# Kernel tuning notes

Measured on AMD Instinct MI355X. Metric: run time of the kernel, lower is better.

The kernel has to match this reference:

```python
import jax, jax.numpy as jnp
import numpy as np

N_NODES = 50000
N_EDGES = 800000
N_REL = 4
F_IN = 128
H1 = 64          # RGCN out
HEADS = 4
D_H = 32         # per-head GAT out
N_GRAPHS = 64


def setup_inputs() -> dict:
    key = jax.random.key(0)
    ks = jax.random.split(key, 16)
    inp = {
        "x": jax.random.normal(ks[0], (N_NODES, F_IN), dtype=jnp.float32),
        "edge_index": jax.random.randint(ks[1], (2, N_EDGES), 0, N_NODES, dtype=jnp.int32),
        "edge_type": jax.random.randint(ks[2], (N_EDGES,), 0, N_REL, dtype=jnp.int32),
        "batch": jnp.sort(jax.random.randint(ks[3], (N_NODES,), 0, N_GRAPHS, dtype=jnp.int32)),
        # RGCNConv params (relation weights, root weight, bias)
        "W_rel": jax.random.normal(ks[4], (N_REL, F_IN, H1), dtype=jnp.float32) * 0.05,
        "W_root": jax.random.normal(ks[5], (F_IN, H1), dtype=jnp.float32) * 0.05,
        "b_rgcn": jnp.zeros((H1,), dtype=jnp.float32),
        # GATConv params
        "W_gat": jax.random.normal(ks[6], (H1, HEADS * D_H), dtype=jnp.float32) * 0.1,
        "att_src": jax.random.normal(ks[7], (HEADS, D_H), dtype=jnp.float32) * 0.1,
        "att_dst": jax.random.normal(ks[8], (HEADS, D_H), dtype=jnp.float32) * 0.1,
        "b_gat": jnp.zeros((HEADS * D_H,), dtype=jnp.float32),
        # dense layers
        "W1": jax.random.normal(ks[9], (HEADS * D_H, 16), dtype=jnp.float32) * 0.05,
        "b1": jnp.zeros((16,), dtype=jnp.float32),
        "W2": jax.random.normal(ks[10], (16, 1), dtype=jnp.float32) * 0.2,
        "b2": jnp.zeros((1,), dtype=jnp.float32),
    }
    return inp


def reference(x, W_rel, W_root, b_rgcn, W_gat, att_src, att_dst, b_gat,
              W1, b1, W2, b2, edge_index, edge_type, batch):
    src, dst = edge_index[0], edge_index[1]
    n = x.shape[0]

    # ---- RGCNConv: mean aggregation per relation, then linear (linearity lets
    # us aggregate raw features first, then apply W_rel) + root transform ----
    xs = x[src]                                            # [E, F_IN]
    out = x @ W_root + b_rgcn                              # [N, H1]
    for r in range(N_REL):
        mask = (edge_type == r).astype(x.dtype)            # [E]
        s = jax.ops.segment_sum(xs * mask[:, None], dst, num_segments=n)
        cnt = jax.ops.segment_sum(mask, dst, num_segments=n)
        mean_r = s / jnp.maximum(cnt, 1.0)[:, None]        # [N, F_IN]
        out = out + mean_r @ W_rel[r]
    h = jax.nn.relu(out)                                   # [N, H1]
    # (dropout omitted: deterministic/eval reference)

    # ---- GATConv (heads=4, concat, no self loops, edge_attr unused) ----
    g = (h @ W_gat).reshape(n, HEADS, D_H)                 # [N, H, D]
    a_s = jnp.einsum('nhd,hd->nh', g, att_src)             # [N, H]
    a_d = jnp.einsum('nhd,hd->nh', g, att_dst)
    e = jax.nn.leaky_relu(a_s[src] + a_d[dst], 0.2)        # [E, H]
    m = jax.ops.segment_max(e, dst, num_segments=n)        # [N, H]
    ex = jnp.exp(e - m[dst])                               # [E, H]
    den = jax.ops.segment_sum(ex, dst, num_segments=n)     # [N, H]
    alpha = ex / den[dst]
    o = jax.ops.segment_sum(alpha[:, :, None] * g[src], dst, num_segments=n)
    o = o.reshape(n, HEADS * D_H) + b_gat                  # [N, 128]
    o = jax.nn.leaky_relu(o, 0.01)

    # ---- dense1 -> leaky_relu -> global max pool -> dense2 ----
    z = jax.nn.leaky_relu(o @ W1 + b1, 0.01)               # [N, 16]
    p = jax.ops.segment_max(z, batch, num_segments=N_GRAPHS)  # [G, 16]
    y = p @ W2 + b2                                        # [G, 1]
    return y
```

## Files before the change

### kernel.cpp

```cpp
#include <hip/hip_runtime.h>
#include <hip/hip_bf16.h>

constexpr int N_NODES = 50000;
constexpr int N_EDGES = 800000;
constexpr int F_IN = 128;
constexpr int H1 = 64;
constexpr int HEADS = 4;
constexpr int D_H = 32;
constexpr int HOUT = HEADS * D_H;
constexpr int N_REL = 4;
constexpr int N_GRAPHS = 64;
constexpr int MBIG = H1 * (1 + N_REL);
constexpr int NBLK = (N_NODES + 255) / 256;
constexpr int N_PAD = 50048;

typedef __attribute__((ext_vector_type(8))) short bf16x8;
typedef __attribute__((ext_vector_type(4))) float f32x4;

__device__ __forceinline__ unsigned f2mono(float f) {
  unsigned u = __float_as_uint(f);
  return (u & 0x80000000u) ? ~u : (u | 0x80000000u);
}
__device__ __forceinline__ float mono2f(unsigned m) {
  unsigned u = (m & 0x80000000u) ? (m & 0x7FFFFFFFu) : ~m;
  return __uint_as_float(u);
}
constexpr unsigned MONO_NEG_INF = 0x007FFFFFu;

__device__ __forceinline__ unsigned short f2bf(float f) {
  unsigned u = __float_as_uint(f);
  unsigned r = (u + 0x7FFFu + ((u >> 16) & 1u)) >> 16;
  return (unsigned short)r;
}
__device__ __forceinline__ float bf2f(unsigned short h) {
  return __uint_as_float((unsigned)h << 16);
}
__device__ __forceinline__ float bflo(unsigned u) { return __uint_as_float(u << 16); }
__device__ __forceinline__ float bfhi(unsigned u) { return __uint_as_float(u & 0xFFFF0000u); }

constexpr int HIST_BLOCKS = (N_EDGES + 255) / 256;
constexpr int WT_BLOCKS = (MBIG * F_IN + HOUT * H1 + 255) / 256;

__global__ __launch_bounds__(256) void pre_fused(
    const float* __restrict__ W_root, const float* __restrict__ W_rel,
    const float* __restrict__ W_gat,
    const float* __restrict__ att_src, const float* __restrict__ att_dst,
    const int* __restrict__ dst,
    unsigned short* __restrict__ WbT_hi, unsigned short* __restrict__ WbT_lo,
    unsigned short* __restrict__ WgT_hi, unsigned short* __restrict__ WgT_lo,
    int* __restrict__ deg, int* __restrict__ rank,
    unsigned* __restrict__ pm,
    float* __restrict__ was, float* __restrict__ wad) {
  int b = blockIdx.x;
  if (b < HIST_BLOCKS) {
    int e = b * 256 + threadIdx.x;
    if (e < N_EDGES) rank[e] = atomicAdd(&deg[dst[e]], 1);
  } else if (b < HIST_BLOCKS + WT_BLOCKS) {
    int i = (b - HIST_BLOCKS) * 256 + threadIdx.x;
    if (i < MBIG * F_IN) {
      int c = i / F_IN, k = i % F_IN;
      float w = (c < H1) ? W_root[k * H1 + c]
                         : W_rel[((size_t)(((c - H1) >> 6) * F_IN + k)) * H1 + ((c - H1) & 63)];
      unsigned short hi = f2bf(w);
      WbT_hi[i] = hi;
      WbT_lo[i] = f2bf(w - bf2f(hi));
    } else {
      int j = i - MBIG * F_IN;
      if (j < HOUT * H1) {
        int c = j / H1, k = j % H1;
        float w = W_gat[k * HOUT + c];
        unsigned short hi = f2bf(w);
        WgT_hi[j] = hi;
        WgT_lo[j] = f2bf(w - bf2f(hi));
      }
    }
  } else if (b == HIST_BLOCKS + WT_BLOCKS) {
    for (int i = threadIdx.x; i < N_GRAPHS * 16; i += 256) pm[i] = MONO_NEG_INF;
  } else {
    int t = threadIdx.x;
    int k = t >> 2, hh = t & 3;
    float s = 0.f, d2 = 0.f;
#pragma unroll 8
    for (int dd = 0; dd < D_H; ++dd) {
      float wg = W_gat[k * HOUT + hh * D_H + dd];
      s += wg * att_src[hh * D_H + dd];
      d2 += wg * att_dst[hh * D_H + dd];
    }
    was[t] = s;
    wad[t] = d2;
  }
}

__device__ __forceinline__ void gemm_body128(int bx, int by,
    const float* __restrict__ Af,
    const unsigned short* __restrict__ BT_hi,
    const unsigned short* __restrict__ BT_lo,
    unsigned short* __restrict__ Cbf, int N, int M) {
  constexpr int K = 128, KC = 64;
  __shared__ unsigned short Ah[64 * KC];
  __shared__ unsigned short Al[64 * KC];
  const int tid = threadIdx.x;
  const int rowBase = bx * 64;
  const int colBase = by * 64;
  const int wv = tid >> 6, lane = tid & 63;
  const int wr = (wv >> 1) * 32, wc = (wv & 1) * 32;
  const int lrow = lane & 15, lkc = lane >> 4;
  int r_[4], c4_[4];
#pragma unroll
  for (int it = 0; it < 4; ++it) {
    int s = it * 256 + tid;
    r_[it] = s >> 4;
    c4_[it] = (s & 15) * 4;
  }
  f32x4 acc[2][2] = {};
#pragma unroll
  for (int it = 0; it < 4; ++it) {
    int gr = rowBase + r_[it];
    float4 v = make_float4(0.f, 0.f, 0.f, 0.f);
    if (gr < N) v = *reinterpret_cast<const float4*>(&Af[(size_t)gr * K + c4_[it]]);
    ushort4 hi, lo;
    hi.x = f2bf(v.x); lo.x = f2bf(v.x - bf2f(hi.x));
    hi.y = f2bf(v.y); lo.y = f2bf(v.y - bf2f(hi.y));
    hi.z = f2bf(v.z); lo.z = f2bf(v.z - bf2f(hi.z));
    hi.w = f2bf(v.w); lo.w = f2bf(v.w - bf2f(hi.w));
    int sw = c4_[it] ^ ((r_[it] & 7) << 3);
    *reinterpret_cast<ushort4*>(&Ah[r_[it] * KC + sw]) = hi;
    *reinterpret_cast<ushort4*>(&Al[r_[it] * KC + sw]) = lo;
  }
  __syncthreads();
  float4 v1[4];
#pragma unroll
  for (int it = 0; it < 4; ++it) {
    int gr = rowBase + r_[it];
    v1[it] = make_float4(0.f, 0.f, 0.f, 0.f);
    if (gr < N) v1[it] = *reinterpret_cast<const float4*>(&Af[(size_t)gr * K + KC + c4_[it]]);
  }
#pragma unroll
  for (int ch = 0; ch < 2; ++ch) {
    if (ch == 1) {
      __syncthreads();
#pragma unroll
      for (int it = 0; it < 4; ++it) {
        float4 v = v1[it];
        ushort4 hi, lo;
        hi.x = f2bf(v.x); lo.x = f2bf(v.x - bf2f(hi.x));
        hi.y = f2bf(v.y); lo.y = f2bf(v.y - bf2f(hi.y));
        hi.z = f2bf(v.z); lo.z = f2bf(v.z - bf2f(hi.z));
        hi.w = f2bf(v.w); lo.w = f2bf(v.w - bf2f(hi.w));
        int sw = c4_[it] ^ ((r_[it] & 7) << 3);
        *reinterpret_cast<ushort4*>(&Ah[r_[it] * KC + sw]) = hi;
        *reinterpret_cast<ushort4*>(&Al[r_[it] * KC + sw]) = lo;
      }
      __syncthreads();
    }
#pragma unroll
    for (int ks = 0; ks < KC; ks += 32) {
      bf16x8 ah[2], al[2], bh[2], bl[2];
#pragma unroll
      for (int fr = 0; fr < 2; ++fr) {
        int r = wr + fr * 16 + lrow;
        int sw = (ks + lkc * 8) ^ ((r & 7) << 3);
        ah[fr] = *reinterpret_cast<const bf16x8*>(&Ah[r * KC + sw]);
        al[fr] = *reinterpret_cast<const bf16x8*>(&Al[r * KC + sw]);
      }
#pragma unroll
      for (int fc = 0; fc < 2; ++fc) {
        int c = colBase + wc + fc * 16 + lrow;
        bh[fc] = *reinterpret_cast<const bf16x8*>(&BT_hi[(size_t)c * K + ch * KC + ks + lkc * 8]);
        bl[fc] = *reinterpret_cast<const bf16x8*>(&BT_lo[(size_t)c * K + ch * KC + ks + lkc * 8]);
      }
#pragma unroll
      for (int fr = 0; fr < 2; ++fr)
#pragma unroll
        for (int fc = 0; fc < 2; ++fc) {
          acc[fr][fc] = __builtin_amdgcn_mfma_f32_16x16x32_bf16(ah[fr], bh[fc], acc[fr][fc], 0, 0, 0);
          acc[fr][fc] = __builtin_amdgcn_mfma_f32_16x16x32_bf16(ah[fr], bl[fc], acc[fr][fc], 0, 0, 0);
          acc[fr][fc] = __builtin_amdgcn_mfma_f32_16x16x32_bf16(al[fr], bh[fc], acc[fr][fc], 0, 0, 0);
        }
    }
  }
#pragma unroll
  for (int fr = 0; fr < 2; ++fr) {
#pragma unroll
    for (int i = 0; i < 4; ++i) {
      int row = rowBase + wr + fr * 16 + lkc * 4 + i;
      if (row < N) {
#pragma unroll
        for (int fc = 0; fc < 2; ++fc) {
          int col = colBase + wc + fc * 16 + lrow;
          Cbf[(size_t)row * M + col] = f2bf(acc[fr][fc][i]);
        }
      }
    }
  }
}

__device__ __forceinline__ void gemm_body64(int bx, int by,
    const unsigned short* __restrict__ Ahi_,
    const unsigned short* __restrict__ Alo_,
    const unsigned short* __restrict__ BT_hi,
    const unsigned short* __restrict__ BT_lo,
    unsigned short* __restrict__ Cbf, int N, int M) {
  constexpr int K = 64;
  __shared__ unsigned short Ah[64 * K];
  __shared__ unsigned short Al[64 * K];
  const int tid = threadIdx.x;
  const int rowBase = bx * 64;
  const int colBase = by * 64;
  constexpr int KQ8 = K / 8;
  for (int s = tid; s < 64 * KQ8; s += 256) {
    int r = s / KQ8, c8 = (s % KQ8) * 8;
    size_t gi = (size_t)(rowBase + r) * K + c8;
    int sw = c8 ^ ((r & 7) << 3);
    *reinterpret_cast<uint4*>(&Ah[r * K + sw]) =
        *reinterpret_cast<const uint4*>(&Ahi_[gi]);
    *reinterpret_cast<uint4*>(&Al[r * K + sw]) =
        *reinterpret_cast<const uint4*>(&Alo_[gi]);
  }
  __syncthreads();
  const int wv = tid >> 6, lane = tid & 63;
  const int wr = (wv >> 1) * 32, wc = (wv & 1) * 32;
  const int lrow = lane & 15, lkc = lane >> 4;
  f32x4 acc[2][2] = {};
#pragma unroll
  for (int ks = 0; ks < K; ks += 32) {
    bf16x8 ah[2], al[2], bh[2], bl[2];
#pragma unroll
    for (int fr = 0; fr < 2; ++fr) {
      int r = wr + fr * 16 + lrow;
      int sw = (ks + lkc * 8) ^ ((r & 7) << 3);
      ah[fr] = *reinterpret_cast<const bf16x8*>(&Ah[r * K + sw]);
      al[fr] = *reinterpret_cast<const bf16x8*>(&Al[r * K + sw]);
    }
#pragma unroll
    for (int fc = 0; fc < 2; ++fc) {
      int c = colBase + wc + fc * 16 + lrow;
      bh[fc] = *reinterpret_cast<const bf16x8*>(&BT_hi[(size_t)c * K + ks + lkc * 8]);
      bl[fc] = *reinterpret_cast<const bf16x8*>(&BT_lo[(size_t)c * K + ks + lkc * 8]);
    }
#pragma unroll
    for (int fr = 0; fr < 2; ++fr)
#pragma unroll
      for (int fc = 0; fc < 2; ++fc) {
        acc[fr][fc] = __builtin_amdgcn_mfma_f32_16x16x32_bf16(ah[fr], bh[fc], acc[fr][fc], 0, 0, 0);
        acc[fr][fc] = __builtin_amdgcn_mfma_f32_16x16x32_bf16(ah[fr], bl[fc], acc[fr][fc], 0, 0, 0);
        acc[fr][fc] = __builtin_amdgcn_mfma_f32_16x16x32_bf16(al[fr], bh[fc], acc[fr][fc], 0, 0, 0);
      }
  }
#pragma unroll
  for (int fr = 0; fr < 2; ++fr) {
#pragma unroll
    for (int i = 0; i < 4; ++i) {
      int row = rowBase + wr + fr * 16 + lkc * 4 + i;
      if (row < N) {
#pragma unroll
        for (int fc = 0; fc < 2; ++fc) {
          int col = colBase + wc + fc * 16 + lrow;
          Cbf[(size_t)row * M + col] = f2bf(acc[fr][fc][i]);
        }
      }
    }
  }
}

constexpr int G1_BX = N_PAD / 64;
constexpr int G1_GRID = 3920;
__global__ __launch_bounds__(256) void gemm1_fill(
    const float* __restrict__ x,
    const unsigned short* __restrict__ wbt_hi, const unsigned short* __restrict__ wbt_lo,
    unsigned short* __restrict__ xtbf,
    const int* __restrict__ src, const int* __restrict__ dst,
    const int* __restrict__ etype, const int* __restrict__ off,
    const int* __restrict__ rank, int* __restrict__ eprep) {
  if (blockIdx.x < G1_GRID) {
    int b = blockIdx.x;
    int r8 = b & 7, s = b >> 3;
    int by = s % 5, q = s / 5;
    int bx = q * 8 + r8;
    if (bx < G1_BX)
      gemm_body128(bx, by, x, wbt_hi, wbt_lo, xtbf, N_NODES, MBIG);
  } else {
    int e = (blockIdx.x - G1_GRID) * 256 + threadIdx.x;
    if (e < N_EDGES) {
      int pos = off[dst[e]] + rank[e];
      eprep[pos] = src[e] | (etype[e] << 16);
    }
  }
}

__global__ __launch_bounds__(256) void gemm2_k(
    const unsigned short* __restrict__ hhi, const unsigned short* __restrict__ hlo,
    const unsigned short* __restrict__ wgt_hi, const unsigned short* __restrict__ wgt_lo,
    unsigned short* __restrict__ gbf) {
  gemm_body64(blockIdx.x % G1_BX, blockIdx.x / G1_BX,
              hhi, hlo, wgt_hi, wgt_lo, gbf, N_NODES, HOUT);
}

__global__ __launch_bounds__(256) void k_s1(const int* __restrict__ deg,
                                            int* __restrict__ bsum) {
  __shared__ int ss[256];
  int t = threadIdx.x;
  int i = blockIdx.x * 256 + t;
  ss[t] = (i < N_NODES) ? deg[i] : 0;
  __syncthreads();
  for (int d = 128; d > 0; d >>= 1) {
    if (t < d) ss[t] += ss[t + d];
    __syncthreads();
  }
  if (t == 0) bsum[blockIdx.x] = ss[0];
}

__global__ __launch_bounds__(256) void k_s2(const int* __restrict__ bsum,
                                            int* __restrict__ bbase,
                                            int* __restrict__ off) {
  __shared__ int ss[256];
  int t = threadIdx.x;
  int v = (t < NBLK) ? bsum[t] : 0;
  ss[t] = v;
  __syncthreads();
  for (int d = 1; d < 256; d <<= 1) {
    int u = (t >= d) ? ss[t - d] : 0;
    __syncthreads();
    ss[t] += u;
    __syncthreads();
  }
  if (t < NBLK) bbase[t] = ss[t] - v;
  if (t == NBLK - 1) off[N_NODES] = ss[t];
}

__global__ __launch_bounds__(256) void k_s3(const int* __restrict__ deg,
                                            const int* __restrict__ bbase,
                                            int* __restrict__ off) {
  __shared__ int ss[256];
  int t = threadIdx.x;
  int i = blockIdx.x * 256 + t;
  int v = (i < N_NODES) ? deg[i] : 0;
  ss[t] = v;
  __syncthreads();
  for (int d = 1; d < 256; d <<= 1) {
    int u = (t >= d) ? ss[t - d] : 0;
    __syncthreads();
    ss[t] += u;
    __syncthreads();
  }
  if (i < N_NODES) off[i] = bbase[blockIdx.x] + ss[t] - v;
}

__global__ __launch_bounds__(256) void rgcn_gather(const unsigned short* __restrict__ xtbf,
                                                   const int* __restrict__ off,
                                                   const int* __restrict__ eprep,
                                                   const float* __restrict__ b_rgcn,
                                                   const float* __restrict__ was,
                                                   const float* __restrict__ wad,
                                                   unsigned short* __restrict__ hhi,
                                                   unsigned short* __restrict__ hlo,
                                                   float* __restrict__ a_s,
                                                   float* __restrict__ a_d) {
  int wid = (blockIdx.x * 256 + threadIdx.x) >> 6;
  int lane = threadIdx.x & 63;
  int half = lane >> 5;
  int cp = lane & 31;
  int start = off[wid], end = off[wid + 1];
  float a0x=0.f,a0y=0.f,a1x=0.f,a1y=0.f,a2x=0.f,a2y=0.f,a3x=0.f,a3y=0.f;
  int c0=0,c1=0,c2=0,c3=0;
  int niter = (end - start + 1) >> 1;
  for (int t = 0; t < niter; t += 2) {
    int idx0 = start + 2 * t + half;
    int idx1 = idx0 + 2;
    int p0 = (idx0 < end) ? eprep[idx0] : 0x70000;
    int p1 = (idx1 < end) ? eprep[idx1] : 0x70000;
    int s0 = p0 & 0xFFFF, r0 = p0 >> 16;
    int s1 = p1 & 0xFFFF, r1 = p1 >> 16;
    unsigned u0 = *reinterpret_cast<const unsigned*>(
        &xtbf[(size_t)s0 * MBIG + H1 + (r0 << 6) + cp * 2]);
    unsigned u1 = *reinterpret_cast<const unsigned*>(
        &xtbf[(size_t)s1 * MBIG + H1 + (r1 << 6) + cp * 2]);
    float v0x = bflo(u0), v0y = bfhi(u0);
    float v1x = bflo(u1), v1y = bfhi(u1);
    a0x += (r0==0)?v0x:0.f; a0y += (r0==0)?v0y:0.f; c0 += (r0==0);
    a1x += (r0==1)?v0x:0.f; a1y += (r0==1)?v0y:0.f; c1 += (r0==1);
    a2x += (r0==2)?v0x:0.f; a2y += (r0==2)?v0y:0.f; c2 += (r0==2);
    a3x += (r0==3)?v0x:0.f; a3y += (r0==3)?v0y:0.f; c3 += (r0==3);
    a0x += (r1==0)?v1x:0.f; a0y += (r1==0)?v1y:0.f; c0 += (r1==0);
    a1x += (r1==1)?v1x:0.f; a1y += (r1==1)?v1y:0.f; c1 += (r1==1);
    a2x += (r1==2)?v1x:0.f; a2y += (r1==2)?v1y:0.f; c2 += (r1==2);
    a3x += (r1==3)?v1x:0.f; a3y += (r1==3)?v1y:0.f; c3 += (r1==3);
  }
  a0x += __shfl_xor(a0x, 32); a0y += __shfl_xor(a0y, 32);
  a1x += __shfl_xor(a1x, 32); a1y += __shfl_xor(a1y, 32);
  a2x += __shfl_xor(a2x, 32); a2y += __shfl_xor(a2y, 32);
  a3x += __shfl_xor(a3x, 32); a3y += __shfl_xor(a3y, 32);
  c0 += __shfl_xor(c0, 32); c1 += __shfl_xor(c1, 32);
  c2 += __shfl_xor(c2, 32); c3 += __shfl_xor(c3, 32);
  if (half == 0) {
    unsigned ur = *reinterpret_cast<const unsigned*>(&xtbf[(size_t)wid * MBIG + cp * 2]);
    float2 bb = *reinterpret_cast<const float2*>(&b_rgcn[cp * 2]);
    float i0 = 1.0f / (float)max(c0, 1);
    float i1 = 1.0f / (float)max(c1, 1);
    float i2 = 1.0f / (float)max(c2, 1);
    float i3 = 1.0f / (float)max(c3, 1);
    float vx = bflo(ur) + bb.x + a0x * i0 + a1x * i1 + a2x * i2 + a3x * i3;
    float vy = bfhi(ur) + bb.y + a0y * i0 + a1y * i1 + a2y * i2 + a3y * i3;
    vx = fmaxf(vx, 0.f);
    vy = fmaxf(vy, 0.f);
    unsigned short hx = f2bf(vx), hy = f2bf(vy);
    ushort2 hv = {hx, hy};
    ushort2 lv = {f2bf(vx - bf2f(hx)), f2bf(vy - bf2f(hy))};
    *reinterpret_cast<ushort2*>(&hhi[(size_t)wid * H1 + cp * 2]) = hv;
    *reinterpret_cast<ushort2*>(&hlo[(size_t)wid * H1 + cp * 2]) = lv;
    float4 wsA = *reinterpret_cast<const float4*>(&was[cp * 8]);
    float4 wsB = *reinterpret_cast<const float4*>(&was[cp * 8 + 4]);
    float4 wdA = *reinterpret_cast<const float4*>(&wad[cp * 8]);
    float4 wdB = *reinterpret_cast<const float4*>(&wad[cp * 8 + 4]);
    float ps0 = vx * wsA.x + vy * wsB.x;
    float ps1 = vx * wsA.y + vy * wsB.y;
    float ps2 = vx * wsA.z + vy * wsB.z;
    float ps3 = vx * wsA.w + vy * wsB.w;
    float pd0 = vx * wdA.x + vy * wdB.x;
    float pd1 = vx * wdA.y + vy * wdB.y;
    float pd2 = vx * wdA.z + vy * wdB.z;
    float pd3 = vx * wdA.w + vy * wdB.w;
#pragma unroll
    for (int d = 1; d < 32; d <<= 1) {
      ps0 += __shfl_xor(ps0, d); ps1 += __shfl_xor(ps1, d);
      ps2 += __shfl_xor(ps2, d); ps3 += __shfl_xor(ps3, d);
      pd0 += __shfl_xor(pd0, d); pd1 += __shfl_xor(pd1, d);
      pd2 += __shfl_xor(pd2, d); pd3 += __shfl_xor(pd3, d);
    }
    if (cp == 0) {
      *reinterpret_cast<float4*>(&a_s[(size_t)wid * 4]) = make_float4(ps0, ps1, ps2, ps3);
      *reinterpret_cast<float4*>(&a_d[(size_t)wid * 4]) = make_float4(pd0, pd1, pd2, pd3);
    }
  }
}

constexpr int GAT_BLOCKS = 2048;
constexpr int GAT_WAVES = GAT_BLOCKS * 4;
__global__ __launch_bounds__(256) void gat_fused(const unsigned short* __restrict__ gbf,
                                                 const float* __restrict__ a_s,
                                                 const float* __restrict__ a_d,
                                                 const int* __restrict__ off,
                                                 const int* __restrict__ eprep,
                                                 const float* __restrict__ b_gat,
                                                 const float* __restrict__ W1,
                                                 const float* __restrict__ b1,
                                                 const int* __restrict__ batch,
                                                 unsigned* __restrict__ p_mono) {
  __shared__ float w1s[HOUT * 16];
  __shared__ float ob[4][HOUT];
  __shared__ unsigned sp[N_GRAPHS * 16];
  const int t = threadIdx.x;
  for (int i = t; i < HOUT * 16; i += 256) w1s[i] = W1[i];
  for (int i = t; i < N_GRAPHS * 16; i += 256) sp[i] = MONO_NEG_INF;
  __syncthreads();
  const int wv = t >> 6, lane = t & 63;
  const int hh = lane >> 4;
  const int jj = lane & 15, grp = lane >> 4;
  const int w = blockIdx.x * 4 + wv;
  const int q = N_NODES / GAT_WAVES;
  const int r = N_NODES % GAT_WAVES;
  const int nbeg = w * q + ((w < r) ? w : r);
  const int ncnt = q + ((w < r) ? 1 : 0);
  for (int wid = nbeg; wid < nbeg + ncnt; ++wid) {
    int start = off[wid], end = off[wid + 1];
    float4 ad4 = *reinterpret_cast<const float4*>(a_d + (size_t)wid * 4);
    float adh = (hh == 0) ? ad4.x : (hh == 1) ? ad4.y : (hh == 2) ? ad4.z : ad4.w;
    float ox = 0.f, oy = 0.f, den = 0.f;
    int i = start;
    for (; i + 4 <= end; i += 4) {
      int p0 = eprep[i], p1 = eprep[i + 1], p2 = eprep[i + 2], p3 = eprep[i + 3];
      int s0 = p0 & 0xFFFF, s1 = p1 & 0xFFFF, s2 = p2 & 0xFFFF, s3 = p3 & 0xFFFF;
      float as0 = a_s[(size_t)s0 * 4 + hh];
      float as1 = a_s[(size_t)s1 * 4 + hh];
      float as2 = a_s[(size_t)s2 * 4 + hh];
      float as3 = a_s[(size_t)s3 * 4 + hh];
      unsigned u0 = *reinterpret_cast<const unsigned*>(&gbf[(size_t)s0 * HOUT + lane * 2]);
      unsigned u1 = *reinterpret_cast<const unsigned*>(&gbf[(size_t)s1 * HOUT + lane * 2]);
      unsigned u2 = *reinterpret_cast<const unsigned*>(&gbf[(size_t)s2 * HOUT + lane * 2]);
      unsigned u3 = *reinterpret_cast<const unsigned*>(&gbf[(size_t)s3 * HOUT + lane * 2]);
      float e0 = as0 + adh; e0 = (e0 > 0.f) ? e0 : 0.2f * e0;
      float e1 = as1 + adh; e1 = (e1 > 0.f) ? e1 : 0.2f * e1;
      float e2 = as2 + adh; e2 = (e2 > 0.f) ? e2 : 0.2f * e2;
      float e3 = as3 + adh; e3 = (e3 > 0.f) ? e3 : 0.2f * e3;
      float x0 = __expf(e0), x1 = __expf(e1), x2 = __expf(e2), x3 = __expf(e3);
      den += x0 + x1 + x2 + x3;
      ox += x0 * bflo(u0) + x1 * bflo(u1) + x2 * bflo(u2) + x3 * bflo(u3);
      oy += x0 * bfhi(u0) + x1 * bfhi(u1) + x2 * bfhi(u2) + x3 * bfhi(u3);
    }
    for (; i < end; ++i) {
      int p = eprep[i];
      int s = p & 0xFFFF;
      float as = a_s[(size_t)s * 4 + hh];
      unsigned u = *reinterpret_cast<const unsigned*>(&gbf[(size_t)s * HOUT + lane * 2]);
      float e = as + adh; e = (e > 0.f) ? e : 0.2f * e;
      float ex = __expf(e);
      den += ex;
      ox += ex * bflo(u);
      oy += ex * bfhi(u);
    }
    float dinv = (den > 0.f) ? (1.0f / den) : 0.f;
    float2 bg = *reinterpret_cast<const float2*>(b_gat + lane * 2);
    float vx = ox * dinv + bg.x; vx = (vx > 0.f) ? vx : 0.01f * vx;
    float vy = oy * dinv + bg.y; vy = (vy > 0.f) ? vy : 0.01f * vy;
    *reinterpret_cast<float2*>(&ob[wv][lane * 2]) = make_float2(vx, vy);
    float acc = 0.f;
#pragma unroll 8
    for (int i2 = 0; i2 < 32; ++i2) {
      int c = grp + 4 * i2;
      acc += ob[wv][c] * w1s[c * 16 + jj];
    }
    acc += __shfl_xor(acc, 16);
    acc += __shfl_xor(acc, 32);
    float z = acc + b1[jj];
    z = (z > 0.f) ? z : 0.01f * z;
    int b = batch[wid];
    if (lane < 16) atomicMax(&sp[b * 16 + jj], f2mono(z));
  }
  __syncthreads();
  for (int i = t; i < N_GRAPHS * 16; i += 256) {
    unsigned v = sp[i];
    if (v != MONO_NEG_INF) atomicMax(p_mono + i, v);
  }
}

__global__ void final_y(const unsigned* __restrict__ p_mono,
                        const float* __restrict__ W2,
                        const float* __restrict__ b2,
                        float* __restrict__ y) {
  int gr = threadIdx.x;
  if (gr >= N_GRAPHS) return;
  float acc = b2[0];
#pragma unroll
  for (int k = 0; k < 16; ++k) acc += mono2f(p_mono[gr * 16 + k]) * W2[k];
  y[gr] = acc;
}

extern "C" void kernel_launch(void* const* d_in, const int* in_sizes, int n_in,
                              void* d_out, int out_size, void* d_ws, size_t ws_size,
                              hipStream_t stream) {
  const float* x       = (const float*)d_in[0];
  const int*   eidx    = (const int*)d_in[1];
  const int*   etype   = (const int*)d_in[2];
  const int*   batch   = (const int*)d_in[3];
  const float* W_rel   = (const float*)d_in[4];
  const float* W_root  = (const float*)d_in[5];
  const float* b_rgcn  = (const float*)d_in[6];
  const float* W_gat   = (const float*)d_in[7];
  const float* att_src = (const float*)d_in[8];
  const float* att_dst = (const float*)d_in[9];
  const float* b_gat   = (const float*)d_in[10];
  const float* W1      = (const float*)d_in[11];
  const float* b1      = (const float*)d_in[12];
  const float* W2      = (const float*)d_in[13];
  const float* b2      = (const float*)d_in[14];
  float* y = (float*)d_out;

  const int* src = eidx;
  const int* dst = eidx + N_EDGES;

  float* ws = (float*)d_ws;
  const size_t OFF_XTBF= 0;
  const size_t OFF_GBF = 0;
  const size_t OFF_HHI = 8007680;
  const size_t OFF_HLO = 9609216;
  const size_t OFF_AS  = 11210752;
  const size_t OFF_AD  = 11410752;
  const size_t OFF_PM  = 11610752;
  const size_t OFF_DEG = 11611776;
  const size_t OFF_OFFS= 11661776;
  const size_t OFF_RANK= 11711780;
  const size_t OFF_EP  = 12511780;
  const size_t OFF_BS  = 13311780;
  const size_t OFF_BB  = 13311976;
  const size_t OFF_WAS = 13312176;
  const size_t OFF_WAD = 13312432;
  const size_t OFF_WBH = 13312688;
  const size_t OFF_WBL = 13333168;
  const size_t OFF_WGH = 13353648;
  const size_t OFF_WGL = 13357744;
  const size_t TOTAL_F = 13361840;
  if (ws_size < TOTAL_F * sizeof(float)) return;

  unsigned short* xtbf = (unsigned short*)(ws + OFF_XTBF);
  unsigned short* gbf  = (unsigned short*)(ws + OFF_GBF);
  unsigned short* hhi  = (unsigned short*)(ws + OFF_HHI);
  unsigned short* hlo  = (unsigned short*)(ws + OFF_HLO);
  float* a_s   = ws + OFF_AS;
  float* a_d   = ws + OFF_AD;
  unsigned* pm = (unsigned*)(ws + OFF_PM);
  int* deg     = (int*)(ws + OFF_DEG);
  int* offs    = (int*)(ws + OFF_OFFS);
  int* rank    = (int*)(ws + OFF_RANK);
  int* eprep   = (int*)(ws + OFF_EP);
  int* bsum    = (int*)(ws + OFF_BS);
  int* bbase   = (int*)(ws + OFF_BB);
  float* was   = ws + OFF_WAS;
  float* wad   = ws + OFF_WAD;
  unsigned short* wbt_hi = (unsigned short*)(ws + OFF_WBH);
  unsigned short* wbt_lo = (unsigned short*)(ws + OFF_WBL);
  unsigned short* wgt_hi = (unsigned short*)(ws + OFF_WGH);
  unsigned short* wgt_lo = (unsigned short*)(ws + OFF_WGL);

  hipMemsetAsync(deg, 0, N_NODES * sizeof(int), stream);

  pre_fused<<<HIST_BLOCKS + WT_BLOCKS + 2, 256, 0, stream>>>(
      W_root, W_rel, W_gat, att_src, att_dst, dst,
      wbt_hi, wbt_lo, wgt_hi, wgt_lo, deg, rank, pm, was, wad);

  k_s1<<<NBLK, 256, 0, stream>>>(deg, bsum);
  k_s2<<<1, 256, 0, stream>>>(bsum, bbase, offs);
  k_s3<<<NBLK, 256, 0, stream>>>(deg, bbase, offs);

  gemm1_fill<<<G1_GRID + HIST_BLOCKS, 256, 0, stream>>>(
      x, wbt_hi, wbt_lo, xtbf, src, dst, etype, offs, rank, eprep);

  rgcn_gather<<<N_NODES / 4, 256, 0, stream>>>(xtbf, offs, eprep, b_rgcn,
                                               was, wad, hhi, hlo, a_s, a_d);

  gemm2_k<<<G1_BX * (HOUT / 64), 256, 0, stream>>>(hhi, hlo, wgt_hi, wgt_lo, gbf);

  gat_fused<<<GAT_BLOCKS, 256, 0, stream>>>(gbf, a_s, a_d, offs, eprep, b_gat,
                                            W1, b1, batch, pm);

  final_y<<<1, 64, 0, stream>>>(pm, W2, b2, y);
}
```

Measured before the change: 208.0 us.

## Fuse GAT linear projection into RGCN gather epilogue, drop separate GEMM

The second GEMM (h @ W_gat) is removed and computed inside rgcn_gather: each wave stores its node's 64-dim h row in LDS, then each lane computes two of the 128 output columns with scalar FMAs, reading the hi/lo bf16 weights from global memory. This avoids writing h as hi/lo bf16 buffers, reading them back, and one kernel launch. In exchange the MFMA GEMM becomes per-node scalar dot products that reread the weight matrix for every node (cache-resident) and lengthen the gather kernel. The gbf buffer moves to its own workspace offset so it no longer aliases xtbf, which is still being read in this kernel.

```diff
diff --git a/kernel.cpp b/kernel.cpp
--- a/kernel.cpp
+++ b/kernel.cpp
@@ -195,74 +195,6 @@
   }
 }
 
-__device__ __forceinline__ void gemm_body64(int bx, int by,
-    const unsigned short* __restrict__ Ahi_,
-    const unsigned short* __restrict__ Alo_,
-    const unsigned short* __restrict__ BT_hi,
-    const unsigned short* __restrict__ BT_lo,
-    unsigned short* __restrict__ Cbf, int N, int M) {
-  constexpr int K = 64;
-  __shared__ unsigned short Ah[64 * K];
-  __shared__ unsigned short Al[64 * K];
-  const int tid = threadIdx.x;
-  const int rowBase = bx * 64;
-  const int colBase = by * 64;
-  constexpr int KQ8 = K / 8;
-  for (int s = tid; s < 64 * KQ8; s += 256) {
-    int r = s / KQ8, c8 = (s % KQ8) * 8;
-    size_t gi = (size_t)(rowBase + r) * K + c8;
-    int sw = c8 ^ ((r & 7) << 3);
-    *reinterpret_cast<uint4*>(&Ah[r * K + sw]) =
-        *reinterpret_cast<const uint4*>(&Ahi_[gi]);
-    *reinterpret_cast<uint4*>(&Al[r * K + sw]) =
-        *reinterpret_cast<const uint4*>(&Alo_[gi]);
-  }
-  __syncthreads();
-  const int wv = tid >> 6, lane = tid & 63;
-  const int wr = (wv >> 1) * 32, wc = (wv & 1) * 32;
-  const int lrow = lane & 15, lkc = lane >> 4;
-  f32x4 acc[2][2] = {};
-#pragma unroll
-  for (int ks = 0; ks < K; ks += 32) {
-    bf16x8 ah[2], al[2], bh[2], bl[2];
-#pragma unroll
-    for (int fr = 0; fr < 2; ++fr) {
-      int r = wr + fr * 16 + lrow;
-      int sw = (ks + lkc * 8) ^ ((r & 7) << 3);
-      ah[fr] = *reinterpret_cast<const bf16x8*>(&Ah[r * K + sw]);
-      al[fr] = *reinterpret_cast<const bf16x8*>(&Al[r * K + sw]);
-    }
-#pragma unroll
-    for (int fc = 0; fc < 2; ++fc) {
-      int c = colBase + wc + fc * 16 + lrow;
-      bh[fc] = *reinterpret_cast<const bf16x8*>(&BT_hi[(size_t)c * K + ks + lkc * 8]);
-      bl[fc] = *reinterpret_cast<const bf16x8*>(&BT_lo[(size_t)c * K + ks + lkc * 8]);
-    }
-#pragma unroll
-    for (int fr = 0; fr < 2; ++fr)
-#pragma unroll
-      for (int fc = 0; fc < 2; ++fc) {
-        acc[fr][fc] = __builtin_amdgcn_mfma_f32_16x16x32_bf16(ah[fr], bh[fc], acc[fr][fc], 0, 0, 0);
-        acc[fr][fc] = __builtin_amdgcn_mfma_f32_16x16x32_bf16(ah[fr], bl[fc], acc[fr][fc], 0, 0, 0);
-        acc[fr][fc] = __builtin_amdgcn_mfma_f32_16x16x32_bf16(al[fr], bh[fc], acc[fr][fc], 0, 0, 0);
-      }
-  }
-#pragma unroll
-  for (int fr = 0; fr < 2; ++fr) {
-#pragma unroll
-    for (int i = 0; i < 4; ++i) {
-      int row = rowBase + wr + fr * 16 + lkc * 4 + i;
-      if (row < N) {
-#pragma unroll
-        for (int fc = 0; fc < 2; ++fc) {
-          int col = colBase + wc + fc * 16 + lrow;
-          Cbf[(size_t)row * M + col] = f2bf(acc[fr][fc][i]);
-        }
-      }
-    }
-  }
-}
-
 constexpr int G1_BX = N_PAD / 64;
 constexpr int G1_GRID = 3920;
 __global__ __launch_bounds__(256) void gemm1_fill(
@@ -288,14 +220,6 @@
   }
 }
 
-__global__ __launch_bounds__(256) void gemm2_k(
-    const unsigned short* __restrict__ hhi, const unsigned short* __restrict__ hlo,
-    const unsigned short* __restrict__ wgt_hi, const unsigned short* __restrict__ wgt_lo,
-    unsigned short* __restrict__ gbf) {
-  gemm_body64(blockIdx.x % G1_BX, blockIdx.x / G1_BX,
-              hhi, hlo, wgt_hi, wgt_lo, gbf, N_NODES, HOUT);
-}
-
 __global__ __launch_bounds__(256) void k_s1(const int* __restrict__ deg,
                                             int* __restrict__ bsum) {
   __shared__ int ss[256];
@@ -352,11 +276,14 @@
                                                    const float* __restrict__ b_rgcn,
                                                    const float* __restrict__ was,
                                                    const float* __restrict__ wad,
-                                                   unsigned short* __restrict__ hhi,
-                                                   unsigned short* __restrict__ hlo,
+                                                   const unsigned short* __restrict__ wgt_hi,
+                                                   const unsigned short* __restrict__ wgt_lo,
+                                                   unsigned short* __restrict__ gbf,
                                                    float* __restrict__ a_s,
                                                    float* __restrict__ a_d) {
+  __shared__ float h_lds[4][H1];
   int wid = (blockIdx.x * 256 + threadIdx.x) >> 6;
+  int wv = threadIdx.x >> 6;
   int lane = threadIdx.x & 63;
   int half = lane >> 5;
   int cp = lane & 31;
@@ -403,11 +330,8 @@
     float vy = bfhi(ur) + bb.y + a0y * i0 + a1y * i1 + a2y * i2 + a3y * i3;
     vx = fmaxf(vx, 0.f);
     vy = fmaxf(vy, 0.f);
-    unsigned short hx = f2bf(vx), hy = f2bf(vy);
-    ushort2 hv = {hx, hy};
-    ushort2 lv = {f2bf(vx - bf2f(hx)), f2bf(vy - bf2f(hy))};
-    *reinterpret_cast<ushort2*>(&hhi[(size_t)wid * H1 + cp * 2]) = hv;
-    *reinterpret_cast<ushort2*>(&hlo[(size_t)wid * H1 + cp * 2]) = lv;
+    h_lds[wv][cp * 2] = vx;
+    h_lds[wv][cp * 2 + 1] = vy;
     float4 wsA = *reinterpret_cast<const float4*>(&was[cp * 8]);
     float4 wsB = *reinterpret_cast<const float4*>(&was[cp * 8 + 4]);
     float4 wdA = *reinterpret_cast<const float4*>(&wad[cp * 8]);
@@ -432,6 +356,29 @@
       *reinterpret_cast<float4*>(&a_d[(size_t)wid * 4]) = make_float4(pd0, pd1, pd2, pd3);
     }
   }
+  __syncthreads();
+  const unsigned short* wh0 = wgt_hi + (size_t)(2 * lane) * H1;
+  const unsigned short* wl0 = wgt_lo + (size_t)(2 * lane) * H1;
+  const unsigned short* wh1 = wh0 + H1;
+  const unsigned short* wl1 = wl0 + H1;
+  float g0 = 0.f, g1 = 0.f;
+#pragma unroll
+  for (int k4 = 0; k4 < H1; k4 += 4) {
+    ushort4 h0 = *reinterpret_cast<const ushort4*>(wh0 + k4);
+    ushort4 l0 = *reinterpret_cast<const ushort4*>(wl0 + k4);
+    ushort4 h1v = *reinterpret_cast<const ushort4*>(wh1 + k4);
+    ushort4 l1v = *reinterpret_cast<const ushort4*>(wl1 + k4);
+    float hk0 = h_lds[wv][k4 + 0];
+    float hk1 = h_lds[wv][k4 + 1];
+    float hk2 = h_lds[wv][k4 + 2];
+    float hk3 = h_lds[wv][k4 + 3];
+    g0 += hk0 * (bf2f(h0.x) + bf2f(l0.x)) + hk1 * (bf2f(h0.y) + bf2f(l0.y))
+        + hk2 * (bf2f(h0.z) + bf2f(l0.z)) + hk3 * (bf2f(h0.w) + bf2f(l0.w));
+    g1 += hk0 * (bf2f(h1v.x) + bf2f(l1v.x)) + hk1 * (bf2f(h1v.y) + bf2f(l1v.y))
+        + hk2 * (bf2f(h1v.z) + bf2f(l1v.z)) + hk3 * (bf2f(h1v.w) + bf2f(l1v.w));
+  }
+  unsigned gp = (unsigned)f2bf(g0) | ((unsigned)f2bf(g1) << 16);
+  *reinterpret_cast<unsigned*>(&gbf[(size_t)wid * HOUT + lane * 2]) = gp;
 }
 
 constexpr int GAT_BLOCKS = 2048;
@@ -560,9 +507,7 @@
 
   float* ws = (float*)d_ws;
   const size_t OFF_XTBF= 0;
-  const size_t OFF_GBF = 0;
-  const size_t OFF_HHI = 8007680;
-  const size_t OFF_HLO = 9609216;
+  const size_t OFF_GBF = 8007680;
   const size_t OFF_AS  = 11210752;
   const size_t OFF_AD  = 11410752;
   const size_t OFF_PM  = 11610752;
@@ -583,8 +528,6 @@
 
   unsigned short* xtbf = (unsigned short*)(ws + OFF_XTBF);
   unsigned short* gbf  = (unsigned short*)(ws + OFF_GBF);
-  unsigned short* hhi  = (unsigned short*)(ws + OFF_HHI);
-  unsigned short* hlo  = (unsigned short*)(ws + OFF_HLO);
   float* a_s   = ws + OFF_AS;
   float* a_d   = ws + OFF_AD;
   unsigned* pm = (unsigned*)(ws + OFF_PM);
@@ -615,9 +558,8 @@
       x, wbt_hi, wbt_lo, xtbf, src, dst, etype, offs, rank, eprep);
 
   rgcn_gather<<<N_NODES / 4, 256, 0, stream>>>(xtbf, offs, eprep, b_rgcn,
-                                               was, wad, hhi, hlo, a_s, a_d);
-
-  gemm2_k<<<G1_BX * (HOUT / 64), 256, 0, stream>>>(hhi, hlo, wgt_hi, wgt_lo, gbf);
+                                               was, wad, wgt_hi, wgt_lo,
+                                               gbf, a_s, a_d);
 
   gat_fused<<<GAT_BLOCKS, 256, 0, stream>>>(gbf, a_s, a_d, offs, eprep, b_gat,
                                             W1, b1, batch, pm);
```

Result: slower. 381.3 us (+83.3%).
